# Kernel tuning notes

Measured on AMD Instinct MI355X. Metric: run time of the kernel, lower is better.

## Reference

```python
import jax, jax.numpy as jnp
import numpy as np

N, D, H, L, E, G, C = 50000, 128, 128, 5, 800000, 512, 10


def setup_inputs() -> dict:
    key = jax.random.key(0)
    ks = jax.random.split(key, 16)
    s = 0.1  # normal init std (Weight_Initializer == 3 style; any init is fine for a math baseline)
    return {
        "x": jax.random.normal(ks[0], (N, D), jnp.float32),
        "edge_index": jax.random.randint(ks[1], (2, E), 0, N, jnp.int32),
        "edge_mask": jax.random.uniform(ks[2], (E,), jnp.float32),
        "batch": jnp.sort(jax.random.randint(ks[3], (N,), 0, G, jnp.int32)),
        "num_graphs": G,
        "eps": jnp.zeros((L,), jnp.float32),
        # per-GIN-layer 2-layer MLP (num_slp_layers=2): D -> H -> D, weights stored [in, out]
        "mlp_w1": jax.random.normal(ks[4], (L, D, H), jnp.float32) * s,
        "mlp_b1": jnp.zeros((L, H), jnp.float32),
        "mlp_w2": jax.random.normal(ks[5], (L, H, D), jnp.float32) * s,
        "mlp_b2": jnp.zeros((L, D), jnp.float32),
        # classifier head: lin1 [(L+1)*D -> (L+1)*D], lin2 [(L+1)*D -> C]
        "lin1_w": jax.random.normal(ks[6], ((L + 1) * D, (L + 1) * D), jnp.float32) * s,
        "lin1_b": jnp.zeros(((L + 1) * D,), jnp.float32),
        "lin2_w": jax.random.normal(ks[7], ((L + 1) * D, C), jnp.float32) * s,
        "lin2_b": jnp.zeros((C,), jnp.float32),
    }


def reference(x, edge_index, edge_mask, batch, num_graphs, eps,
              mlp_w1, mlp_b1, mlp_w2, mlp_b2, lin1_w, lin1_b, lin2_w, lin2_b):
    n = x.shape[0]
    src, dst = edge_index[0], edge_index[1]
    embeds = [x]
    h = x
    for l in range(eps.shape[0]):
        # A @ h with A[src,dst] = edge_mask: gather neighbor feats, weight, scatter-add to src
        agg = jax.ops.segment_sum(edge_mask[:, None] * h[dst], src, num_segments=n)  # [N,D]
        pooled = agg + (1.0 + eps[l]) * h
        h1 = jax.nn.relu(pooled @ mlp_w1[l] + mlp_b1[l])
        h = jax.nn.relu(h1 @ mlp_w2[l] + mlp_b2[l])
        embeds.append(h)
    stacked = jnp.stack(embeds)  # [L+1, N, D]
    # global_add_pool per layer, then per-graph concat across layers -> [G, (L+1)*D]
    pooled_g = jax.vmap(lambda e: jax.ops.segment_sum(e, batch, num_segments=num_graphs))(stacked)
    merged = jnp.transpose(pooled_g, (1, 0, 2)).reshape(num_graphs, -1)
    lin1_out = jax.nn.relu(merged @ lin1_w + lin1_b)  # dropout p=0 -> identity
    lin2_out = lin1_out @ lin2_w + lin2_b
    return jax.nn.softmax(lin2_out, axis=1)  # [G, C]
```

## Files before the change

kernel.cpp:

```cpp
#include <hip/hip_runtime.h>


typedef __bf16 bf16x8 __attribute__((ext_vector_type(8)));
typedef float f32x4 __attribute__((ext_vector_type(4)));

static inline int ceil_div(int a, int b) { return (a + b - 1) / b; }

__device__ inline ushort bf_rne(float v) {
  unsigned u = __float_as_uint(v);
  return (ushort)((u + 0x7fffu + ((u >> 16) & 1u)) >> 16);
}
__device__ inline float bf2f(ushort u) { return __uint_as_float((unsigned)u << 16); }
__device__ inline float bf2f_lo(unsigned g) { return __uint_as_float(g << 16); }
__device__ inline float bf2f_hi(unsigned g) { return __uint_as_float(g & 0xffff0000u); }

__global__ void k_hist(const int* __restrict__ src, int* __restrict__ deg, int E) {
  int i = blockIdx.x * blockDim.x + threadIdx.x;
  if (i < E) atomicAdd(&deg[src[i]], 1);
}

__global__ __launch_bounds__(256) void k_scan1(const int* __restrict__ deg,
                                               int* __restrict__ excl,
                                               int* __restrict__ bsum, int N) {
  __shared__ int tsum[256];
  int b = blockIdx.x, t = threadIdx.x;
  int base = b * 1024 + t * 4;
  int v0 = 0, v1 = 0, v2 = 0, v3 = 0;
  if (base + 3 < N) {
    int4 q = *(const int4*)&deg[base];
    v0 = q.x; v1 = q.y; v2 = q.z; v3 = q.w;
  } else {
    if (base + 0 < N) v0 = deg[base + 0];
    if (base + 1 < N) v1 = deg[base + 1];
    if (base + 2 < N) v2 = deg[base + 2];
    if (base + 3 < N) v3 = deg[base + 3];
  }
  tsum[t] = v0 + v1 + v2 + v3;
  __syncthreads();
  for (int off = 1; off < 256; off <<= 1) {
    int x = (t >= off) ? tsum[t - off] : 0;
    __syncthreads();
    tsum[t] += x;
    __syncthreads();
  }
  int pre = (t == 0) ? 0 : tsum[t - 1];
  if (base < N)     excl[base]     = pre;
  if (base + 1 < N) excl[base + 1] = pre + v0;
  if (base + 2 < N) excl[base + 2] = pre + v0 + v1;
  if (base + 3 < N) excl[base + 3] = pre + v0 + v1 + v2;
  if (t == 255) bsum[b] = tsum[255];
}

__global__ __launch_bounds__(256) void k_scan3(const int* __restrict__ excl,
                                               const int* __restrict__ bsum, int nb,
                                               int* __restrict__ rowptr,
                                               int* __restrict__ cursor, int N) {
  __shared__ int s[256];
  int t = threadIdx.x;
  s[t] = (t < nb) ? bsum[t] : 0;
  __syncthreads();
  for (int off = 1; off < 256; off <<= 1) {
    int x = (t >= off) ? s[t - off] : 0;
    __syncthreads();
    s[t] += x;
    __syncthreads();
  }
  int i = blockIdx.x * 256 + t;
  if (i < N) {
    int blk = i >> 10;
    int boff = blk ? s[blk - 1] : 0;
    int v = excl[i] + boff;
    rowptr[i] = v;
    cursor[i] = v;
  }
  if (i == N - 1) rowptr[N] = s[nb - 1];
}

__global__ void k_scatter(const int* __restrict__ src, const int* __restrict__ dst,
                          const float* __restrict__ mask, int* __restrict__ cursor,
                          int2* __restrict__ sedge, int E) {
  int i = blockIdx.x * blockDim.x + threadIdx.x;
  if (i < E) {
    int s = src[i];
    int p = atomicAdd(&cursor[s], 1);
    sedge[p] = make_int2(dst[i], __float_as_int(mask[i]));
  }
}

__global__ __launch_bounds__(256) void k_tobf16(const float* __restrict__ in,
                                                ushort* __restrict__ out, int n) {
  int base = (blockIdx.x * 256 + threadIdx.x) * 4;
  if (base + 3 < n) {
    float4 v = *(const float4*)&in[base];
    ushort4 o;
    o.x = bf_rne(v.x); o.y = bf_rne(v.y); o.z = bf_rne(v.z); o.w = bf_rne(v.w);
    *(ushort4*)&out[base] = o;
  } else {
    for (int k = base; k < n; ++k) out[k] = bf_rne(in[k]);
  }
}

__global__ __launch_bounds__(256) void k_prep_all(
    const float* __restrict__ W1, const float* __restrict__ W2,
    const float* __restrict__ L1W,
    ushort* __restrict__ hi1, ushort* __restrict__ hi2,
    ushort* __restrict__ l1hi, ushort* __restrict__ l1lo, int L, int F) {
  __shared__ float t[32][33];
  int z = blockIdx.z;
  int tx = threadIdx.x & 31, ty = threadIdx.x >> 5;
  if (z < 2 * L) {
    if (blockIdx.x >= 4 || blockIdx.y >= 4) return;
    const float* Wm = (z < L) ? (W1 + (size_t)z * 128 * 128)
                              : (W2 + (size_t)(z - L) * 128 * 128);
    ushort* him = (z < L) ? (hi1 + (size_t)z * 128 * 128)
                          : (hi2 + (size_t)(z - L) * 128 * 128);
    int k0 = blockIdx.x * 32, n0 = blockIdx.y * 32;
#pragma unroll
    for (int r = 0; r < 32; r += 8)
      t[ty + r][tx] = Wm[(size_t)(k0 + ty + r) * 128 + n0 + tx];
    __syncthreads();
#pragma unroll
    for (int r = 0; r < 32; r += 8)
      him[(size_t)(n0 + ty + r) * 128 + k0 + tx] = bf_rne(t[tx][ty + r]);
  } else {
    int k0 = blockIdx.x * 32, n0 = blockIdx.y * 32;
#pragma unroll
    for (int r = 0; r < 32; r += 8)
      t[ty + r][tx] = L1W[(size_t)(k0 + ty + r) * F + n0 + tx];
    __syncthreads();
#pragma unroll
    for (int r = 0; r < 32; r += 8) {
      float v = t[tx][ty + r];
      size_t o = (size_t)(n0 + ty + r) * F + k0 + tx;
      ushort h = bf_rne(v);
      l1hi[o] = h;
      l1lo[o] = bf_rne(v - bf2f(h));
    }
  }
}

__global__ __launch_bounds__(128) void k_agg(const ushort* __restrict__ h,
                                             const int* __restrict__ rowptr,
                                             const int2* __restrict__ sedge,
                                             const float* __restrict__ eps, int layer,
                                             ushort* __restrict__ pooled, int N) {
  int v = blockIdx.x * 2 + (threadIdx.x >> 6);
  int lane = threadIdx.x & 63;
  if (v >= N) return;
  int beg = rowptr[v], end = rowptr[v + 1];
  float ax[8] = {}, ay[8] = {};
  int j = beg;
  for (; j + 8 <= end; j += 8) {
    long long e[8];
    unsigned g[8];
#pragma unroll
    for (int q = 0; q < 8; ++q)
      e[q] = __builtin_nontemporal_load((const long long*)(sedge + j + q));
#pragma unroll
    for (int q = 0; q < 8; ++q) {
      int d = (int)(unsigned)e[q];
      g[q] = *(const unsigned*)&h[(size_t)d * 128 + lane * 2];
    }
#pragma unroll
    for (int q = 0; q < 8; ++q) {
      float m = __int_as_float((int)(e[q] >> 32));
      ax[q] = fmaf(m, bf2f_lo(g[q]), ax[q]);
      ay[q] = fmaf(m, bf2f_hi(g[q]), ay[q]);
    }
  }
  for (; j + 2 <= end; j += 2) {
    long long e0 = __builtin_nontemporal_load((const long long*)(sedge + j));
    long long e1 = __builtin_nontemporal_load((const long long*)(sedge + j + 1));
    unsigned g0 = *(const unsigned*)&h[(size_t)(int)(unsigned)e0 * 128 + lane * 2];
    unsigned g1 = *(const unsigned*)&h[(size_t)(int)(unsigned)e1 * 128 + lane * 2];
    float m0 = __int_as_float((int)(e0 >> 32));
    float m1 = __int_as_float((int)(e1 >> 32));
    ax[0] = fmaf(m0, bf2f_lo(g0), ax[0]);
    ay[0] = fmaf(m0, bf2f_hi(g0), ay[0]);
    ax[1] = fmaf(m1, bf2f_lo(g1), ax[1]);
    ay[1] = fmaf(m1, bf2f_hi(g1), ay[1]);
  }
  if (j < end) {
    long long e = __builtin_nontemporal_load((const long long*)(sedge + j));
    unsigned g = *(const unsigned*)&h[(size_t)(int)(unsigned)e * 128 + lane * 2];
    float m = __int_as_float((int)(e >> 32));
    ax[0] = fmaf(m, bf2f_lo(g), ax[0]);
    ay[0] = fmaf(m, bf2f_hi(g), ay[0]);
  }
  float sx = ((ax[0] + ax[1]) + (ax[2] + ax[3])) + ((ax[4] + ax[5]) + (ax[6] + ax[7]));
  float sy = ((ay[0] + ay[1]) + (ay[2] + ay[3])) + ((ay[4] + ay[5]) + (ay[6] + ay[7]));
  float ep = 1.0f + eps[layer];
  unsigned gs = *(const unsigned*)&h[(size_t)v * 128 + lane * 2];
  sx = fmaf(ep, bf2f_lo(gs), sx);
  sy = fmaf(ep, bf2f_hi(gs), sy);
  unsigned outw = (unsigned)bf_rne(sx) | ((unsigned)bf_rne(sy) << 16);
  __builtin_nontemporal_store(outw, (unsigned*)&pooled[(size_t)v * 128 + lane * 2]);
}

__global__ __launch_bounds__(256) void k_mlp(
    const ushort* __restrict__ pooled,
    const ushort* __restrict__ w1t, const float* __restrict__ b1,
    const ushort* __restrict__ w2t, const float* __restrict__ b2,
    ushort* __restrict__ hout, int N) {
  __shared__ ushort Ws[128][128];
  __shared__ ushort H1s[64][128];
  int tid = threadIdx.x;
  int w = tid >> 6, lane = tid & 63;
  int row0 = blockIdx.x * 64;
  int wr = w >> 1, wc = w & 1;

#pragma unroll
  for (int i = 0; i < 8; ++i) {
    int f = i * 256 + tid;
    int r = f >> 4, c8 = (f & 15) * 8;
    *(bf16x8*)&Ws[r][c8 ^ ((r & 7) << 3)] = *(const bf16x8*)&w1t[(size_t)r * 128 + c8];
  }
  bf16x8 w2r[8];
#pragma unroll
  for (int i = 0; i < 8; ++i) {
    int f = i * 256 + tid;
    int r = f >> 4, c8 = (f & 15) * 8;
    w2r[i] = *(const bf16x8*)&w2t[(size_t)r * 128 + c8];
  }
  __syncthreads();

  f32x4 acc[2][4];
#pragma unroll
  for (int m = 0; m < 2; ++m)
#pragma unroll
    for (int n = 0; n < 4; ++n) acc[m][n] = (f32x4){0.f, 0.f, 0.f, 0.f};
#pragma unroll
  for (int ks = 0; ks < 4; ++ks) {
    int kk = ks * 32 + (lane >> 4) * 8;
    bf16x8 a[2], b[4];
#pragma unroll
    for (int m = 0; m < 2; ++m) {
      int arow = row0 + wr * 32 + m * 16 + (lane & 15);
      if (arow >= N) arow = N - 1;
      a[m] = *(const bf16x8*)&pooled[(size_t)arow * 128 + kk];
    }
#pragma unroll
    for (int n = 0; n < 4; ++n) {
      int r = wc * 64 + n * 16 + (lane & 15);
      b[n] = *(bf16x8*)&Ws[r][kk ^ ((r & 7) << 3)];
    }
#pragma unroll
    for (int m = 0; m < 2; ++m)
#pragma unroll
      for (int n = 0; n < 4; ++n)
        acc[m][n] = __builtin_amdgcn_mfma_f32_16x16x32_bf16(a[m], b[n], acc[m][n], 0, 0, 0);
  }
#pragma unroll
  for (int m = 0; m < 2; ++m) {
    int rbase = wr * 32 + m * 16 + (lane >> 4) * 4;
#pragma unroll
    for (int n = 0; n < 4; ++n) {
      int col = wc * 64 + n * 16 + (lane & 15);
      float bb = b1[col];
#pragma unroll
      for (int r = 0; r < 4; ++r) {
        int row = rbase + r;
        float v = fmaxf(acc[m][n][r] + bb, 0.f);
        H1s[row][col ^ ((row & 7) << 3)] = bf_rne(v);
      }
    }
  }
  __syncthreads();

#pragma unroll
  for (int i = 0; i < 8; ++i) {
    int f = i * 256 + tid;
    int r = f >> 4, c8 = (f & 15) * 8;
    *(bf16x8*)&Ws[r][c8 ^ ((r & 7) << 3)] = w2r[i];
  }
  __syncthreads();

#pragma unroll
  for (int m = 0; m < 2; ++m)
#pragma unroll
    for (int n = 0; n < 4; ++n) acc[m][n] = (f32x4){0.f, 0.f, 0.f, 0.f};
#pragma unroll
  for (int ks = 0; ks < 4; ++ks) {
    int kk = ks * 32 + (lane >> 4) * 8;
    bf16x8 a[2], b[4];
#pragma unroll
    for (int m = 0; m < 2; ++m) {
      int r = wr * 32 + m * 16 + (lane & 15);
      a[m] = *(bf16x8*)&H1s[r][kk ^ ((r & 7) << 3)];
    }
#pragma unroll
    for (int n = 0; n < 4; ++n) {
      int r = wc * 64 + n * 16 + (lane & 15);
      b[n] = *(bf16x8*)&Ws[r][kk ^ ((r & 7) << 3)];
    }
#pragma unroll
    for (int m = 0; m < 2; ++m)
#pragma unroll
      for (int n = 0; n < 4; ++n)
        acc[m][n] = __builtin_amdgcn_mfma_f32_16x16x32_bf16(a[m], b[n], acc[m][n], 0, 0, 0);
  }
#pragma unroll
  for (int m = 0; m < 2; ++m) {
    int rbase = row0 + wr * 32 + m * 16 + (lane >> 4) * 4;
#pragma unroll
    for (int n = 0; n < 4; ++n) {
      int col = wc * 64 + n * 16 + (lane & 15);
      float bb = b2[col];
#pragma unroll
      for (int r = 0; r < 4; ++r) {
        int row = rbase + r;
        if (row < N) {
          float v = fmaxf(acc[m][n][r] + bb, 0.f);
          hout[(size_t)row * 128 + col] = bf_rne(v);
        }
      }
    }
  }
}

template <int RELU, int OUT_BF16, int SPLITW>
__global__ __launch_bounds__(256) void k_mgemm(const ushort* __restrict__ A,
                                               const ushort* __restrict__ Wt_hi,
                                               const ushort* __restrict__ Wt_lo,
                                               const float* __restrict__ bias,
                                               void* __restrict__ Cout,
                                               int M, int N, int K) {
  __shared__ ushort As[64][128];
  __shared__ ushort Ws_hi[64][128];
  __shared__ ushort Ws_lo[SPLITW ? 64 : 1][SPLITW ? 128 : 1];
  int tid = threadIdx.x;
  int row0 = blockIdx.y * 64, col0 = blockIdx.x * 64;
  int w = tid >> 6, lane = tid & 63;
  int wr = w >> 1, wc = w & 1;
  f32x4 acc[2][2] = {};
  int nk = K >> 7;
  for (int kc = 0; kc < nk; ++kc) {
    int k0 = kc << 7;
    if (kc) __syncthreads();
#pragma unroll
    for (int i = 0; i < 4; ++i) {
      int f = i * 256 + tid;
      int r = f >> 4, c8 = (f & 15) * 8;
      int ksw = c8 ^ ((r & 7) << 3);
      if (row0 + r < M) {
        *(bf16x8*)&As[r][ksw] = *(const bf16x8*)&A[(size_t)(row0 + r) * K + k0 + c8];
      } else {
        ushort4 z = {0, 0, 0, 0};
        *(ushort4*)&As[r][ksw] = z;
        *(ushort4*)&As[r][ksw + 4] = z;
      }
    }
#pragma unroll
    for (int i = 0; i < 4; ++i) {
      int f = i * 256 + tid;
      int r = f >> 4, c8 = (f & 15) * 8;
      int ksw = c8 ^ ((r & 7) << 3);
      *(bf16x8*)&Ws_hi[r][ksw] = *(const bf16x8*)&Wt_hi[(size_t)(col0 + r) * K + k0 + c8];
      if (SPLITW)
        *(bf16x8*)&Ws_lo[r][ksw] = *(const bf16x8*)&Wt_lo[(size_t)(col0 + r) * K + k0 + c8];
    }
    __syncthreads();
#pragma unroll
    for (int ks = 0; ks < 4; ++ks) {
      int kk = ks * 32 + (lane >> 4) * 8;
      bf16x8 a[2], bh[2], bl[2];
#pragma unroll
      for (int m = 0; m < 2; ++m) {
        int r = wr * 32 + m * 16 + (lane & 15);
        a[m] = *(bf16x8*)&As[r][kk ^ ((r & 7) << 3)];
      }
#pragma unroll
      for (int n = 0; n < 2; ++n) {
        int r = wc * 32 + n * 16 + (lane & 15);
        int ksw = kk ^ ((r & 7) << 3);
        bh[n] = *(bf16x8*)&Ws_hi[r][ksw];
        if (SPLITW) bl[n] = *(bf16x8*)&Ws_lo[r][ksw];
      }
#pragma unroll
      for (int m = 0; m < 2; ++m)
#pragma unroll
        for (int n = 0; n < 2; ++n) {
          acc[m][n] = __builtin_amdgcn_mfma_f32_16x16x32_bf16(a[m], bh[n], acc[m][n], 0, 0, 0);
          if (SPLITW)
            acc[m][n] = __builtin_amdgcn_mfma_f32_16x16x32_bf16(a[m], bl[n], acc[m][n], 0, 0, 0);
        }
    }
  }
#pragma unroll
  for (int m = 0; m < 2; ++m) {
    int rbase = row0 + wr * 32 + m * 16 + (lane >> 4) * 4;
#pragma unroll
    for (int n = 0; n < 2; ++n) {
      int col = col0 + wc * 32 + n * 16 + (lane & 15);
      float b = bias[col];
#pragma unroll
      for (int r = 0; r < 4; ++r) {
        int row = rbase + r;
        if (row < M) {
          float v = acc[m][n][r] + b;
          if (RELU) v = fmaxf(v, 0.f);
          if (OUT_BF16)
            ((ushort*)Cout)[(size_t)row * N + col] = bf_rne(v);
          else
            ((float*)Cout)[(size_t)row * N + col] = v;
        }
      }
    }
  }
}

__global__ __launch_bounds__(128) void k_pool_all(
    const ushort* __restrict__ f0, const ushort* __restrict__ f1,
    const ushort* __restrict__ f2, const ushort* __restrict__ f3,
    const ushort* __restrict__ f4, const ushort* __restrict__ f5,
    const int* __restrict__ batch, ushort* __restrict__ pg, int N, int L1) {
  __shared__ float red[2][64][2];
  int g = blockIdx.x;
  int slot = blockIdx.y;
  const ushort* feat;
  switch (slot) {
    case 0: feat = f0; break;
    case 1: feat = f1; break;
    case 2: feat = f2; break;
    case 3: feat = f3; break;
    case 4: feat = f4; break;
    default: feat = f5; break;
  }
  int w = threadIdx.x >> 6, lane = threadIdx.x & 63;
  int lo = 0, hi = N;
  while (lo < hi) {
    int mid = (lo + hi) >> 1;
    if (batch[mid] < g) lo = mid + 1; else hi = mid;
  }
  int s = lo;
  hi = N;
  while (lo < hi) {
    int mid = (lo + hi) >> 1;
    if (batch[mid] < g + 1) lo = mid + 1; else hi = mid;
  }
  int e = lo;
  float a0 = 0.f, a1 = 0.f;
#pragma unroll 4
  for (int v = s + w; v < e; v += 2) {
    unsigned u = __builtin_nontemporal_load((const unsigned*)&feat[(size_t)v * 128 + lane * 2]);
    a0 += bf2f_lo(u);
    a1 += bf2f_hi(u);
  }
  red[w][lane][0] = a0;
  red[w][lane][1] = a1;
  __syncthreads();
  if (w == 0) {
    a0 = red[0][lane][0] + red[1][lane][0];
    a1 = red[0][lane][1] + red[1][lane][1];
    unsigned outw = (unsigned)bf_rne(a0) | ((unsigned)bf_rne(a1) << 16);
    *(unsigned*)&pg[((size_t)g * L1 + slot) * 128 + lane * 2] = outw;
  }
}

__global__ __launch_bounds__(64) void k_lin2_softmax(const float* __restrict__ A,
                                                     const float* __restrict__ W,
                                                     const float* __restrict__ b,
                                                     float* __restrict__ out, int K, int C) {
  constexpr int CMAX = 16;
  int g = blockIdx.x;
  int lane = threadIdx.x;
  float acc[CMAX];
#pragma unroll
  for (int c = 0; c < CMAX; ++c) acc[c] = 0.f;
  for (int k = lane; k < K; k += 64) {
    float a = A[(size_t)g * K + k];
#pragma unroll
    for (int c = 0; c < CMAX; ++c)
      if (c < C) acc[c] = fmaf(a, W[(size_t)k * C + c], acc[c]);
  }
#pragma unroll
  for (int off = 32; off; off >>= 1)
#pragma unroll
    for (int c = 0; c < CMAX; ++c) acc[c] += __shfl_xor(acc[c], off, 64);
  if (lane == 0) {
    float mx = -3.0e38f;
#pragma unroll
    for (int c = 0; c < CMAX; ++c)
      if (c < C) {
        acc[c] += b[c];
        mx = fmaxf(mx, acc[c]);
      }
    float sum = 0.f;
#pragma unroll
    for (int c = 0; c < CMAX; ++c)
      if (c < C) {
        acc[c] = expf(acc[c] - mx);
        sum += acc[c];
      }
    float inv = 1.f / sum;
#pragma unroll
    for (int c = 0; c < CMAX; ++c)
      if (c < C) out[(size_t)g * C + c] = acc[c] * inv;
  }
}

extern "C" void kernel_launch(void* const* d_in, const int* in_sizes, int n_in,
                              void* d_out, int out_size, void* d_ws, size_t ws_size,
                              hipStream_t stream) {
  const float* x     = (const float*)d_in[0];
  const int*   eidx  = (const int*)d_in[1];
  const float* emask = (const float*)d_in[2];
  const int*   batch = (const int*)d_in[3];
  const float* eps   = (const float*)d_in[5];
  const float* w1    = (const float*)d_in[6];
  const float* b1    = (const float*)d_in[7];
  const float* w2    = (const float*)d_in[8];
  const float* b2    = (const float*)d_in[9];
  const float* l1w   = (const float*)d_in[10];
  const float* l1b   = (const float*)d_in[11];
  const float* l2w   = (const float*)d_in[12];
  const float* l2b   = (const float*)d_in[13];

  const int N = in_sizes[3];
  const int E = in_sizes[2];
  const int L = in_sizes[5];
  const int D = in_sizes[0] / N;
  const int C = in_sizes[13];
  const int G = out_size / C;
  const int L1 = L + 1;
  const int H = in_sizes[7] / L;
  const int F = L1 * D;

  const int* src = eidx;
  const int* dst = eidx + E;

  char* p = (char*)d_ws;
  auto carve = [&](size_t bytes) -> void* {
    void* r = (void*)p;
    p += (bytes + 255) & ~(size_t)255;
    return r;
  };
  int*    rowptr = (int*)carve((size_t)(N + 1) * 4);
  int*    cursor = (int*)carve((size_t)N * 4);
  int*    deg    = (int*)carve((size_t)N * 4);
  int*    excl   = (int*)carve((size_t)N * 4);
  int*    bsum   = (int*)carve(256 * 4);
  int2*   sedge  = (int2*)carve((size_t)E * 8);
  ushort* xb     = (ushort*)carve((size_t)N * D * 2);
  ushort* pooled = (ushort*)carve((size_t)N * D * 2);
  ushort* hb[5];
  for (int l = 0; l < 5; ++l) hb[l] = (ushort*)carve((size_t)N * D * 2);
  ushort* pg     = (ushort*)carve((size_t)G * F * 2);
  float*  l1out  = (float*)carve((size_t)G * F * 4);
  ushort* w1t_hi = (ushort*)carve((size_t)L * D * H * 2);
  ushort* w2t_hi = (ushort*)carve((size_t)L * H * D * 2);
  ushort* l1t_hi = (ushort*)carve((size_t)F * F * 2);
  ushort* l1t_lo = (ushort*)carve((size_t)F * F * 2);
  (void)ws_size;

  const int nb = ceil_div(N, 1024);
  hipMemsetAsync(deg, 0, (size_t)N * 4, stream);
  k_hist<<<ceil_div(E, 256), 256, 0, stream>>>(src, deg, E);
  k_scan1<<<nb, 256, 0, stream>>>(deg, excl, bsum, N);
  k_scan3<<<ceil_div(N, 256), 256, 0, stream>>>(excl, bsum, nb, rowptr, cursor, N);
  k_scatter<<<ceil_div(E, 256), 256, 0, stream>>>(src, dst, emask, cursor, sedge, E);

  k_tobf16<<<ceil_div(N * D, 1024), 256, 0, stream>>>(x, xb, N * D);
  k_prep_all<<<dim3(F / 32, F / 32, 2 * L + 1), 256, 0, stream>>>(
      w1, w2, l1w, w1t_hi, w2t_hi, l1t_hi, l1t_lo, L, F);

  const ushort* h_in = xb;
  for (int l = 0; l < L; ++l) {
    k_agg<<<ceil_div(N, 2), 128, 0, stream>>>(h_in, rowptr, sedge, eps, l, pooled, N);
    k_mlp<<<ceil_div(N, 64), 256, 0, stream>>>(
        pooled, w1t_hi + (size_t)l * D * H, b1 + (size_t)l * H,
        w2t_hi + (size_t)l * H * D, b2 + (size_t)l * D, hb[l], N);
    h_in = hb[l];
  }

  k_pool_all<<<dim3(G, L1), 128, 0, stream>>>(xb, hb[0], hb[1], hb[2], hb[3], hb[4],
                                              batch, pg, N, L1);

  k_mgemm<1, 0, 1><<<dim3(F / 64, ceil_div(G, 64)), 256, 0, stream>>>(
      pg, l1t_hi, l1t_lo, l1b, l1out, G, F, F);
  k_lin2_softmax<<<G, 64, 0, stream>>>(l1out, l2w, l2b, (float*)d_out, F, C);
}
```

Before: 459.7 us.

## Replace CSR edge scatter with two-pass bucketed scatter; drop nontemporal hints

```diff
diff --git a/kernel.cpp b/kernel.cpp
--- a/kernel.cpp
+++ b/kernel.cpp
@@ -54,7 +54,7 @@
 __global__ __launch_bounds__(256) void k_scan3(const int* __restrict__ excl,
                                                const int* __restrict__ bsum, int nb,
                                                int* __restrict__ rowptr,
-                                               int* __restrict__ cursor, int N) {
+                                               int* __restrict__ bcursor, int N) {
   __shared__ int s[256];
   int t = threadIdx.x;
   s[t] = (t < nb) ? bsum[t] : 0;
@@ -71,19 +71,79 @@
     int boff = blk ? s[blk - 1] : 0;
     int v = excl[i] + boff;
     rowptr[i] = v;
-    cursor[i] = v;
+    if ((i & 511) == 0) bcursor[i >> 9] = v;
   }
   if (i == N - 1) rowptr[N] = s[nb - 1];
 }
 
-__global__ void k_scatter(const int* __restrict__ src, const int* __restrict__ dst,
-                          const float* __restrict__ mask, int* __restrict__ cursor,
-                          int2* __restrict__ sedge, int E) {
-  int i = blockIdx.x * blockDim.x + threadIdx.x;
-  if (i < E) {
-    int s = src[i];
-    int p = atomicAdd(&cursor[s], 1);
-    sedge[p] = make_int2(dst[i], __float_as_int(mask[i]));
+__global__ __launch_bounds__(256) void k_scat_a(
+    const int* __restrict__ src, const int* __restrict__ dst,
+    const float* __restrict__ mask, int* __restrict__ bcursor,
+    int4* __restrict__ bsedge, int E, int nbuck) {
+  __shared__ int hist[128], basep[128], lcur[128], runst[128];
+  __shared__ int4 stage[2048];
+  int tid = threadIdx.x;
+  int e0 = blockIdx.x * 2048;
+  int ecnt = min(2048, E - e0);
+  for (int b = tid; b < nbuck; b += 256) hist[b] = 0;
+  __syncthreads();
+  int s[8], d[8], m[8];
+#pragma unroll
+  for (int q = 0; q < 8; ++q) {
+    int idx = tid + q * 256;
+    if (idx < ecnt) {
+      s[q] = src[e0 + idx];
+      d[q] = dst[e0 + idx];
+      m[q] = __float_as_int(mask[e0 + idx]);
+      atomicAdd(&hist[s[q] >> 9], 1);
+    }
+  }
+  __syncthreads();
+  if (tid == 0) {
+    int run = 0;
+    for (int b = 0; b < nbuck; ++b) {
+      basep[b] = run;
+      run += hist[b];
+    }
+  }
+  __syncthreads();
+  for (int b = tid; b < nbuck; b += 256) lcur[b] = basep[b];
+  __syncthreads();
+#pragma unroll
+  for (int q = 0; q < 8; ++q) {
+    int idx = tid + q * 256;
+    if (idx < ecnt) {
+      int b = s[q] >> 9;
+      int slot = atomicAdd(&lcur[b], 1);
+      stage[slot] = make_int4(s[q], d[q], m[q], b);
+    }
+  }
+  __syncthreads();
+  for (int b = tid; b < nbuck; b += 256)
+    runst[b] = hist[b] ? atomicAdd(&bcursor[b], hist[b]) : 0;
+  __syncthreads();
+  for (int slot = tid; slot < ecnt; slot += 256) {
+    int4 e = stage[slot];
+    int pos = runst[e.w] + (slot - basep[e.w]);
+    bsedge[pos] = e;
+  }
+}
+
+__global__ __launch_bounds__(256) void k_scat_b(
+    const int4* __restrict__ bsedge, const int* __restrict__ rowptr,
+    int2* __restrict__ sedge, int N) {
+  __shared__ int cur[512];
+  int b = blockIdx.x;
+  int n0 = b << 9;
+  int n1 = min(n0 + 512, N);
+  int tid = threadIdx.x;
+  for (int i = tid; i < n1 - n0; i += 256) cur[i] = rowptr[n0 + i];
+  __syncthreads();
+  int e0 = rowptr[n0], e1 = rowptr[n1];
+  for (int j = e0 + tid; j < e1; j += 256) {
+    int4 e = bsedge[j];
+    int p = atomicAdd(&cur[e.x - n0], 1);
+    sedge[p] = make_int2(e.y, e.z);
   }
 }
 
@@ -151,39 +211,33 @@
   float ax[8] = {}, ay[8] = {};
   int j = beg;
   for (; j + 8 <= end; j += 8) {
-    long long e[8];
+    int2 e[8];
     unsigned g[8];
 #pragma unroll
+    for (int q = 0; q < 8; ++q) e[q] = sedge[j + q];
+#pragma unroll
     for (int q = 0; q < 8; ++q)
-      e[q] = __builtin_nontemporal_load((const long long*)(sedge + j + q));
+      g[q] = *(const unsigned*)&h[(size_t)e[q].x * 128 + lane * 2];
 #pragma unroll
     for (int q = 0; q < 8; ++q) {
-      int d = (int)(unsigned)e[q];
-      g[q] = *(const unsigned*)&h[(size_t)d * 128 + lane * 2];
-    }
-#pragma unroll
-    for (int q = 0; q < 8; ++q) {
-      float m = __int_as_float((int)(e[q] >> 32));
+      float m = __int_as_float(e[q].y);
       ax[q] = fmaf(m, bf2f_lo(g[q]), ax[q]);
       ay[q] = fmaf(m, bf2f_hi(g[q]), ay[q]);
     }
   }
   for (; j + 2 <= end; j += 2) {
-    long long e0 = __builtin_nontemporal_load((const long long*)(sedge + j));
-    long long e1 = __builtin_nontemporal_load((const long long*)(sedge + j + 1));
-    unsigned g0 = *(const unsigned*)&h[(size_t)(int)(unsigned)e0 * 128 + lane * 2];
-    unsigned g1 = *(const unsigned*)&h[(size_t)(int)(unsigned)e1 * 128 + lane * 2];
-    float m0 = __int_as_float((int)(e0 >> 32));
-    float m1 = __int_as_float((int)(e1 >> 32));
-    ax[0] = fmaf(m0, bf2f_lo(g0), ax[0]);
-    ay[0] = fmaf(m0, bf2f_hi(g0), ay[0]);
-    ax[1] = fmaf(m1, bf2f_lo(g1), ax[1]);
-    ay[1] = fmaf(m1, bf2f_hi(g1), ay[1]);
+    int2 e0 = sedge[j], e1 = sedge[j + 1];
+    unsigned g0 = *(const unsigned*)&h[(size_t)e0.x * 128 + lane * 2];
+    unsigned g1 = *(const unsigned*)&h[(size_t)e1.x * 128 + lane * 2];
+    ax[0] = fmaf(__int_as_float(e0.y), bf2f_lo(g0), ax[0]);
+    ay[0] = fmaf(__int_as_float(e0.y), bf2f_hi(g0), ay[0]);
+    ax[1] = fmaf(__int_as_float(e1.y), bf2f_lo(g1), ax[1]);
+    ay[1] = fmaf(__int_as_float(e1.y), bf2f_hi(g1), ay[1]);
   }
   if (j < end) {
-    long long e = __builtin_nontemporal_load((const long long*)(sedge + j));
-    unsigned g = *(const unsigned*)&h[(size_t)(int)(unsigned)e * 128 + lane * 2];
-    float m = __int_as_float((int)(e >> 32));
+    int2 e = sedge[j];
+    unsigned g = *(const unsigned*)&h[(size_t)e.x * 128 + lane * 2];
+    float m = __int_as_float(e.y);
     ax[0] = fmaf(m, bf2f_lo(g), ax[0]);
     ay[0] = fmaf(m, bf2f_hi(g), ay[0]);
   }
@@ -194,7 +248,7 @@
   sx = fmaf(ep, bf2f_lo(gs), sx);
   sy = fmaf(ep, bf2f_hi(gs), sy);
   unsigned outw = (unsigned)bf_rne(sx) | ((unsigned)bf_rne(sy) << 16);
-  __builtin_nontemporal_store(outw, (unsigned*)&pooled[(size_t)v * 128 + lane * 2]);
+  *(unsigned*)&pooled[(size_t)v * 128 + lane * 2] = outw;
 }
 
 __global__ __launch_bounds__(256) void k_mlp(
@@ -215,13 +269,6 @@
     int r = f >> 4, c8 = (f & 15) * 8;
     *(bf16x8*)&Ws[r][c8 ^ ((r & 7) << 3)] = *(const bf16x8*)&w1t[(size_t)r * 128 + c8];
   }
-  bf16x8 w2r[8];
-#pragma unroll
-  for (int i = 0; i < 8; ++i) {
-    int f = i * 256 + tid;
-    int r = f >> 4, c8 = (f & 15) * 8;
-    w2r[i] = *(const bf16x8*)&w2t[(size_t)r * 128 + c8];
-  }
   __syncthreads();
 
   f32x4 acc[2][4];
@@ -271,7 +318,7 @@
   for (int i = 0; i < 8; ++i) {
     int f = i * 256 + tid;
     int r = f >> 4, c8 = (f & 15) * 8;
-    *(bf16x8*)&Ws[r][c8 ^ ((r & 7) << 3)] = w2r[i];
+    *(bf16x8*)&Ws[r][c8 ^ ((r & 7) << 3)] = *(const bf16x8*)&w2t[(size_t)r * 128 + c8];
   }
   __syncthreads();
 
@@ -442,7 +489,7 @@
   float a0 = 0.f, a1 = 0.f;
 #pragma unroll 4
   for (int v = s + w; v < e; v += 2) {
-    unsigned u = __builtin_nontemporal_load((const unsigned*)&feat[(size_t)v * 128 + lane * 2]);
+    unsigned u = *(const unsigned*)&feat[(size_t)v * 128 + lane * 2];
     a0 += bf2f_lo(u);
     a1 += bf2f_hi(u);
   }
@@ -535,30 +582,33 @@
     p += (bytes + 255) & ~(size_t)255;
     return r;
   };
-  int*    rowptr = (int*)carve((size_t)(N + 1) * 4);
-  int*    cursor = (int*)carve((size_t)N * 4);
-  int*    deg    = (int*)carve((size_t)N * 4);
-  int*    excl   = (int*)carve((size_t)N * 4);
-  int*    bsum   = (int*)carve(256 * 4);
-  int2*   sedge  = (int2*)carve((size_t)E * 8);
-  ushort* xb     = (ushort*)carve((size_t)N * D * 2);
-  ushort* pooled = (ushort*)carve((size_t)N * D * 2);
+  int*    rowptr  = (int*)carve((size_t)(N + 1) * 4);
+  int*    deg     = (int*)carve((size_t)N * 4);
+  int*    excl    = (int*)carve((size_t)N * 4);
+  int*    bsum    = (int*)carve(256 * 4);
+  int*    bcursor = (int*)carve(256 * 4);
+  int2*   sedge   = (int2*)carve((size_t)E * 8);
+  int4*   bsedge  = (int4*)carve((size_t)E * 16);
+  ushort* xb      = (ushort*)carve((size_t)N * D * 2);
+  ushort* pooled  = (ushort*)carve((size_t)N * D * 2);
   ushort* hb[5];
   for (int l = 0; l < 5; ++l) hb[l] = (ushort*)carve((size_t)N * D * 2);
-  ushort* pg     = (ushort*)carve((size_t)G * F * 2);
-  float*  l1out  = (float*)carve((size_t)G * F * 4);
-  ushort* w1t_hi = (ushort*)carve((size_t)L * D * H * 2);
-  ushort* w2t_hi = (ushort*)carve((size_t)L * H * D * 2);
-  ushort* l1t_hi = (ushort*)carve((size_t)F * F * 2);
-  ushort* l1t_lo = (ushort*)carve((size_t)F * F * 2);
+  ushort* pg      = (ushort*)carve((size_t)G * F * 2);
+  float*  l1out   = (float*)carve((size_t)G * F * 4);
+  ushort* w1t_hi  = (ushort*)carve((size_t)L * D * H * 2);
+  ushort* w2t_hi  = (ushort*)carve((size_t)L * H * D * 2);
+  ushort* l1t_hi  = (ushort*)carve((size_t)F * F * 2);
+  ushort* l1t_lo  = (ushort*)carve((size_t)F * F * 2);
   (void)ws_size;
 
   const int nb = ceil_div(N, 1024);
+  const int nbuck = ceil_div(N, 512);
   hipMemsetAsync(deg, 0, (size_t)N * 4, stream);
   k_hist<<<ceil_div(E, 256), 256, 0, stream>>>(src, deg, E);
   k_scan1<<<nb, 256, 0, stream>>>(deg, excl, bsum, N);
-  k_scan3<<<ceil_div(N, 256), 256, 0, stream>>>(excl, bsum, nb, rowptr, cursor, N);
-  k_scatter<<<ceil_div(E, 256), 256, 0, stream>>>(src, dst, emask, cursor, sedge, E);
+  k_scan3<<<ceil_div(N, 256), 256, 0, stream>>>(excl, bsum, nb, rowptr, bcursor, N);
+  k_scat_a<<<ceil_div(E, 2048), 256, 0, stream>>>(src, dst, emask, bcursor, bsedge, E, nbuck);
+  k_scat_b<<<nbuck, 256, 0, stream>>>(bsedge, rowptr, sedge, N);
 
   k_tobf16<<<ceil_div(N * D, 1024), 256, 0, stream>>>(x, xb, N * D);
   k_prep_all<<<dim3(F / 32, F / 32, 2 * L + 1), 256, 0, stream>>>(
```

After: 401.9 us (median of 2 runs). -12.6%, faster.
